# Kernel optimization log

Measured on AMD Instinct MI355X. Metric: run time of the kernel, lower is better.

## Reference

```python
import jax, jax.numpy as jnp
import numpy as np

TOP_K = 2
NUM_EXPERTS = 8

def setup_inputs() -> dict:
    key = jax.random.key(0)
    k_x, k_r, k_g, k_u, k_d = jax.random.split(key, 5)
    B, L, D, H, E = 1, 2048, 1024, 2048, NUM_EXPERTS
    scale = 0.02  # keep router logits / activations in a sane range
    return {
        "x": jax.random.normal(k_x, (B, L, D), dtype=jnp.float32),
        "router_w": jax.random.normal(k_r, (D, E), dtype=jnp.float32) * scale,
        "gate_w": jax.random.normal(k_g, (E, D, H), dtype=jnp.float32) * scale,
        "up_w": jax.random.normal(k_u, (E, D, H), dtype=jnp.float32) * scale,
        "down_w": jax.random.normal(k_d, (E, H, D), dtype=jnp.float32) * scale,
    }

def reference(x, router_w, gate_w, up_w, down_w):
    # x: (B, L, D)
    B, L, D = x.shape
    T = B * L
    E = router_w.shape[1]
    xf = x.reshape(T, D)

    # --- router: top-k softmax over selected logits (Mixtral-style) ---
    logits = xf @ router_w                      # (T, E)
    top_vals, top_idx = jax.lax.top_k(logits, TOP_K)  # (T, K)
    top_w = jax.nn.softmax(top_vals, axis=-1)   # (T, K)

    # combine weights scattered to dense (T, E); zeros for unrouted experts
    combine = jnp.zeros((T, E), dtype=x.dtype).at[
        jnp.arange(T)[:, None], top_idx
    ].add(top_w)

    # --- experts: SwiGLU, computed per expert, zero-weight tokens masked by combine ---
    gate = jnp.einsum('td,edh->eth', xf, gate_w)   # (E, T, H)
    up = jnp.einsum('td,edh->eth', xf, up_w)       # (E, T, H)
    hidden = jax.nn.silu(gate) * up                # (E, T, H)
    expert_out = jnp.einsum('eth,ehd->etd', hidden, down_w)  # (E, T, D)

    # --- weighted combine (equivalent to scatter_add over sorted assignments) ---
    y = jnp.einsum('etd,te->td', expert_out, combine)  # (T, D)
    return y.reshape(B, L, D)
```

## Files before the change

### kernel.cpp

```cpp
#include <hip/hip_runtime.h>
#include <hip/hip_bf16.h>
#include <stdint.h>

#define T_TOK 2048
#define DIM   1024
#define HDIM  2048
#define NE    8
#define ROWS_PAD 4224

typedef __attribute__((ext_vector_type(8))) short bf16x8;
typedef __attribute__((ext_vector_type(4))) float f32x4;

__device__ __forceinline__ unsigned short f2bf(float f) {
    union { float f; unsigned int u; } v; v.f = f;
    unsigned int r = v.u + 0x7FFF + ((v.u >> 16) & 1);
    return (unsigned short)(r >> 16);
}

__device__ __forceinline__ void gload16(const void* g, void* l) {
    __builtin_amdgcn_global_load_lds(
        (const __attribute__((address_space(1))) void*)g,
        (__attribute__((address_space(3))) void*)l, 16, 0, 0);
}

__global__ void transpose_cvt(const float* __restrict__ in, unsigned short* __restrict__ out,
                              int R, int C) {
    __shared__ float tile[32][33];
    int b = blockIdx.z;
    int bx = blockIdx.x, by = blockIdx.y;
    int tx = threadIdx.x & 31, ty = threadIdx.x >> 5;
    const float* ip = in + (size_t)b * R * C;
    unsigned short* op = out + (size_t)b * R * C;
#pragma unroll
    for (int i = 0; i < 4; ++i) {
        int r = by * 32 + ty + i * 8;
        tile[ty + i * 8][tx] = ip[(size_t)r * C + bx * 32 + tx];
    }
    __syncthreads();
#pragma unroll
    for (int i = 0; i < 4; ++i) {
        int oc = bx * 32 + ty + i * 8;
        int orw = by * 32 + tx;
        op[(size_t)oc * R + orw] = f2bf(tile[tx][ty + i * 8]);
    }
}

__global__ void router_kernel(const float* __restrict__ x, const float* __restrict__ rw,
                              int* __restrict__ counts, int* __restrict__ top_idx,
                              float* __restrict__ top_w) {
    int wid = (blockIdx.x * blockDim.x + threadIdx.x) >> 6;
    int lane = threadIdx.x & 63;
    if (wid >= T_TOK) return;
    float acc[NE];
#pragma unroll
    for (int e = 0; e < NE; ++e) acc[e] = 0.f;
    const float* xr = x + (size_t)wid * DIM;
    for (int i = lane; i < DIM; i += 64) {
        float xv = xr[i];
        const float* wr = rw + (size_t)i * NE;
#pragma unroll
        for (int e = 0; e < NE; ++e) acc[e] += xv * wr[e];
    }
#pragma unroll
    for (int off = 32; off; off >>= 1) {
#pragma unroll
        for (int e = 0; e < NE; ++e) acc[e] += __shfl_xor(acc[e], off, 64);
    }
    if (lane == 0) {
        float v0 = -1e30f, v1 = -1e30f; int i0 = 0, i1 = 0;
#pragma unroll
        for (int e = 0; e < NE; ++e) {
            float v = acc[e];
            if (v > v0) { v1 = v0; i1 = i0; v0 = v; i0 = e; }
            else if (v > v1) { v1 = v; i1 = e; }
        }
        float e1 = __expf(v1 - v0);
        float s = 1.f + e1;
        top_idx[wid * 2]     = i0;
        top_idx[wid * 2 + 1] = i1;
        top_w[wid * 2]     = 1.f / s;
        top_w[wid * 2 + 1] = e1 / s;
        atomicAdd(&counts[i0], 1);
        atomicAdd(&counts[i1], 1);
    }
}

__global__ void scan_kernel(const int* __restrict__ counts, int* __restrict__ offsets,
                            int* __restrict__ cursors) {
    if (threadIdx.x == 0) {
        int run = 0;
        for (int e = 0; e < NE; ++e) { offsets[e] = run; cursors[e] = run; run += counts[e]; }
    }
}

__global__ void gather_kernel(const float* __restrict__ x, const int* __restrict__ top_idx,
                              const float* __restrict__ top_w, int* __restrict__ cursors,
                              int* __restrict__ row_tok, float* __restrict__ row_w,
                              unsigned short* __restrict__ Abuf) {
    int t = blockIdx.x;
    __shared__ int pos[2];
    if (threadIdx.x < 2) {
        int k = threadIdx.x;
        int e = top_idx[t * 2 + k];
        int p = atomicAdd(&cursors[e], 1);
        pos[k] = p;
        row_tok[p] = t;
        row_w[p] = top_w[t * 2 + k];
    }
    __syncthreads();
    const float4* xr = (const float4*)(x + (size_t)t * DIM);
    float4 v = xr[threadIdx.x];
    ushort4 b;
    b.x = f2bf(v.x); b.y = f2bf(v.y); b.z = f2bf(v.z); b.w = f2bf(v.w);
    ushort4* A4 = (ushort4*)Abuf;
    A4[(size_t)pos[0] * (DIM / 4) + threadIdx.x] = b;
    A4[(size_t)pos[1] * (DIM / 4) + threadIdx.x] = b;
}

__global__ __launch_bounds__(256, 2)
void gemm1_kernel(const unsigned short* __restrict__ Abuf,
                  const unsigned short* __restrict__ WgT,
                  const unsigned short* __restrict__ WuT,
                  unsigned short* __restrict__ Hbuf,
                  const int* __restrict__ offsets, const int* __restrict__ counts) {
    const int e = blockIdx.z;
    const int cnt = counts[e];
    const int mtile = blockIdx.y;
    if (mtile * 128 >= cnt) return;
    const int n0 = blockIdx.x * 128;
    const int row0 = offsets[e] + mtile * 128;

    __shared__ unsigned short As[2][128 * 32];
    __shared__ unsigned short Bg[2][128 * 32];
    __shared__ unsigned short Bu[2][128 * 32];

    const int tid = threadIdx.x;
    const int lane = tid & 63;
    const int wave = tid >> 6;
    const int wm = wave >> 1, wn = wave & 1;

    f32x4 accg[4][4], accu[4][4];
#pragma unroll
    for (int i = 0; i < 4; ++i)
#pragma unroll
        for (int j = 0; j < 4; ++j) {
            accg[i][j] = (f32x4){0.f, 0.f, 0.f, 0.f};
            accu[i][j] = (f32x4){0.f, 0.f, 0.f, 0.f};
        }

    const int srow0 = tid >> 2;
    const int sc0 = tid & 3;
    const unsigned short* Aab = Abuf + (size_t)row0 * DIM;
    const unsigned short* Bgb = WgT + (size_t)e * HDIM * DIM + (size_t)n0 * DIM;
    const unsigned short* Bub = WuT + (size_t)e * HDIM * DIM + (size_t)n0 * DIM;

    auto stage = [&](int buf, int kt) {
#pragma unroll
        for (int i = 0; i < 2; ++i) {
            int row = i * 64 + srow0;
            int csrc = sc0 ^ ((row >> 1) & 3);
            size_t go = (size_t)row * DIM + kt + csrc * 8;
            int lo = (i * 256 + tid) * 8;
            gload16(Aab + go, &As[buf][lo]);
            gload16(Bgb + go, &Bg[buf][lo]);
            gload16(Bub + go, &Bu[buf][lo]);
        }
    };

    const int rsel = lane & 15;
    const int csrcf = lane >> 4;

    stage(0, 0);
    int cur = 0;
    for (int kt = 0; kt < DIM; kt += 32) {
        __syncthreads();
        if (kt + 32 < DIM) stage(cur ^ 1, kt + 32);
        const unsigned short* Ac = As[cur];
        const unsigned short* Bgc = Bg[cur];
        const unsigned short* Buc = Bu[cur];
        bf16x8 af[4], bg[4], bu[4];
#pragma unroll
        for (int i = 0; i < 4; ++i) {
            int ra = wm * 64 + i * 16 + rsel;
            af[i] = *(const bf16x8*)&Ac[ra * 32 + (csrcf ^ ((ra >> 1) & 3)) * 8];
            int rb = wn * 64 + i * 16 + rsel;
            int cb = (csrcf ^ ((rb >> 1) & 3)) * 8;
            bg[i] = *(const bf16x8*)&Bgc[rb * 32 + cb];
            bu[i] = *(const bf16x8*)&Buc[rb * 32 + cb];
        }
#pragma unroll
        for (int i = 0; i < 4; ++i)
#pragma unroll
            for (int j = 0; j < 4; ++j) {
                accg[i][j] = __builtin_amdgcn_mfma_f32_16x16x32_bf16(af[i], bg[j], accg[i][j], 0, 0, 0);
                accu[i][j] = __builtin_amdgcn_mfma_f32_16x16x32_bf16(af[i], bu[j], accu[i][j], 0, 0, 0);
            }
        cur ^= 1;
    }

    const int c = lane & 15, rbase = (lane >> 4) * 4;
    const int obase = offsets[e];
#pragma unroll
    for (int i = 0; i < 4; ++i) {
#pragma unroll
        for (int r = 0; r < 4; ++r) {
            int lrow = mtile * 128 + wm * 64 + i * 16 + rbase + r;
            if (lrow < cnt) {
                size_t orow = (size_t)(obase + lrow);
#pragma unroll
                for (int j = 0; j < 4; ++j) {
                    float g = accg[i][j][r], u = accu[i][j][r];
                    float h = g * u / (1.f + __expf(-g));
                    Hbuf[orow * HDIM + n0 + wn * 64 + j * 16 + c] = f2bf(h);
                }
            }
        }
    }
}

__global__ __launch_bounds__(256, 2)
void gemm2_kernel(const unsigned short* __restrict__ Hbuf,
                  const unsigned short* __restrict__ WdT,
                  float* __restrict__ y,
                  const int* __restrict__ offsets, const int* __restrict__ counts,
                  const int* __restrict__ row_tok, const float* __restrict__ row_w) {
    const int e = blockIdx.z >> 1;
    const int kc = blockIdx.z & 1;
    const int cnt = counts[e];
    const int mtile = blockIdx.y;
    if (mtile * 128 >= cnt) return;
    const int n0 = blockIdx.x * 128;
    const int row0 = offsets[e] + mtile * 128;

    __shared__ unsigned short As[2][128 * 64];
    __shared__ unsigned short Bs[2][128 * 64];

    const int tid = threadIdx.x;
    const int lane = tid & 63;
    const int wave = tid >> 6;
    const int wm = wave >> 1, wn = wave & 1;

    f32x4 acc[4][4];
#pragma unroll
    for (int i = 0; i < 4; ++i)
#pragma unroll
        for (int j = 0; j < 4; ++j) acc[i][j] = (f32x4){0.f, 0.f, 0.f, 0.f};

    const int srow0 = tid >> 3;
    const int sc0 = tid & 7;
    const unsigned short* Aab = Hbuf + (size_t)row0 * HDIM;
    const unsigned short* Bbb = WdT + (size_t)e * DIM * HDIM + (size_t)n0 * HDIM;

    auto stage = [&](int buf, int kt) {
#pragma unroll
        for (int i = 0; i < 4; ++i) {
            int row = i * 32 + srow0;
            int csrc = sc0 ^ (row & 7);
            size_t go = (size_t)row * HDIM + kt + csrc * 8;
            int lo = (i * 256 + tid) * 8;
            gload16(Aab + go, &As[buf][lo]);
            gload16(Bbb + go, &Bs[buf][lo]);
        }
    };

    const int rsel = lane & 15;
    const int csrcf = lane >> 4;

    const int kbeg = kc * (HDIM / 2);
    const int kend = kbeg + (HDIM / 2);

    stage(0, kbeg);
    int cur = 0;
    for (int kt = kbeg; kt < kend; kt += 64) {
        __syncthreads();
        if (kt + 64 < kend) stage(cur ^ 1, kt + 64);
        const unsigned short* Ac = As[cur];
        const unsigned short* Bc = Bs[cur];
#pragma unroll
        for (int kk = 0; kk < 2; ++kk) {
            bf16x8 af[4], bf[4];
#pragma unroll
            for (int i = 0; i < 4; ++i) {
                int ra = wm * 64 + i * 16 + rsel;
                af[i] = *(const bf16x8*)&Ac[ra * 64 + ((kk * 4 + csrcf) ^ (ra & 7)) * 8];
                int rb = wn * 64 + i * 16 + rsel;
                bf[i] = *(const bf16x8*)&Bc[rb * 64 + ((kk * 4 + csrcf) ^ (rb & 7)) * 8];
            }
#pragma unroll
            for (int i = 0; i < 4; ++i)
#pragma unroll
                for (int j = 0; j < 4; ++j)
                    acc[i][j] = __builtin_amdgcn_mfma_f32_16x16x32_bf16(af[i], bf[j], acc[i][j], 0, 0, 0);
        }
        cur ^= 1;
    }

    const int c = lane & 15, rbase = (lane >> 4) * 4;
    const int obase = offsets[e];
#pragma unroll
    for (int i = 0; i < 4; ++i) {
#pragma unroll
        for (int r = 0; r < 4; ++r) {
            int lrow = mtile * 128 + wm * 64 + i * 16 + rbase + r;
            if (lrow < cnt) {
                int grow = obase + lrow;
                int tok = row_tok[grow];
                float w = row_w[grow];
#pragma unroll
                for (int j = 0; j < 4; ++j) {
                    atomicAdd(&y[(size_t)tok * DIM + n0 + wn * 64 + j * 16 + c], w * acc[i][j][r]);
                }
            }
        }
    }
}

extern "C" void kernel_launch(void* const* d_in, const int* in_sizes, int n_in,
                              void* d_out, int out_size, void* d_ws, size_t ws_size,
                              hipStream_t stream) {
    const float* x  = (const float*)d_in[0];
    const float* rw = (const float*)d_in[1];
    const float* gw = (const float*)d_in[2];
    const float* uw = (const float*)d_in[3];
    const float* dw = (const float*)d_in[4];
    float* y = (float*)d_out;

    char* ws = (char*)d_ws;
    int*   counts  = (int*)(ws + 0);
    int*   cursors = (int*)(ws + 32);
    int*   offsets = (int*)(ws + 64);
    int*   top_idx = (int*)(ws + 128);
    float* top_w   = (float*)(ws + 128 + 16384);
    int*   row_tok = (int*)(ws + 128 + 32768);
    float* row_w   = (float*)(ws + 128 + 32768 + 16896);
    size_t off = 128 + 32768 + 2 * 16896;
    off = (off + 255) & ~(size_t)255;
    unsigned short* Abuf = (unsigned short*)(ws + off); off += (size_t)ROWS_PAD * DIM * 2;
    unsigned short* Hbuf = (unsigned short*)(ws + off); off += (size_t)ROWS_PAD * HDIM * 2;
    unsigned short* WgT  = (unsigned short*)(ws + off); off += (size_t)NE * DIM * HDIM * 2;
    unsigned short* WuT  = (unsigned short*)(ws + off); off += (size_t)NE * DIM * HDIM * 2;
    unsigned short* WdT  = (unsigned short*)(ws + off); off += (size_t)NE * DIM * HDIM * 2;
    if (ws_size < off) return;

    hipMemsetAsync(counts, 0, 32, stream);
    hipMemsetAsync(d_out, 0, (size_t)out_size * 4, stream);

    transpose_cvt<<<dim3(HDIM / 32, DIM / 32, NE), 256, 0, stream>>>(gw, WgT, DIM, HDIM);
    transpose_cvt<<<dim3(HDIM / 32, DIM / 32, NE), 256, 0, stream>>>(uw, WuT, DIM, HDIM);
    transpose_cvt<<<dim3(DIM / 32, HDIM / 32, NE), 256, 0, stream>>>(dw, WdT, HDIM, DIM);

    router_kernel<<<T_TOK / 4, 256, 0, stream>>>(x, rw, counts, top_idx, top_w);
    scan_kernel<<<1, 64, 0, stream>>>(counts, offsets, cursors);
    gather_kernel<<<T_TOK, 256, 0, stream>>>(x, top_idx, top_w, cursors, row_tok, row_w, Abuf);

    gemm1_kernel<<<dim3(HDIM / 128, 16, NE), 256, 0, stream>>>(Abuf, WgT, WuT, Hbuf, offsets, counts);
    gemm2_kernel<<<dim3(DIM / 128, 16, NE * 2), 256, 0, stream>>>(Hbuf, WdT, y, offsets, counts, row_tok, row_w);
}
```

Before: 281.9 us.

## Triple-buffer LDS pipelines in both expert GEMMs with explicit vmcnt waits

Both expert GEMM kernels move from double to triple buffering of shared-memory tiles. Two stages are prefetched ahead, and each iteration waits with an explicit s_waitcnt vmcnt count plus a raw barrier instead of __syncthreads, so global-to-LDS loads can overlap more compute. gemm2 also shrinks its K tile from 64 to 32, which lowers its LDS footprint, and raises its launch bounds to 3 blocks per SM for higher occupancy. Risks: the hand-set vmcnt counts rely on the compiler not adding other outstanding vector memory ops, and the smaller K step in gemm2 doubles the barrier count.

After: 285.5 us. About the same (+1.3%).

```diff
diff --git a/kernel.cpp b/kernel.cpp
--- a/kernel.cpp
+++ b/kernel.cpp
@@ -130,9 +130,9 @@
     const int n0 = blockIdx.x * 128;
     const int row0 = offsets[e] + mtile * 128;
 
-    __shared__ unsigned short As[2][128 * 32];
-    __shared__ unsigned short Bg[2][128 * 32];
-    __shared__ unsigned short Bu[2][128 * 32];
+    __shared__ unsigned short As[3][128 * 32];
+    __shared__ unsigned short Bg[3][128 * 32];
+    __shared__ unsigned short Bu[3][128 * 32];
 
     const int tid = threadIdx.x;
     const int lane = tid & 63;
@@ -170,11 +170,18 @@
     const int rsel = lane & 15;
     const int csrcf = lane >> 4;
 
+    const int NS = DIM / 32;
     stage(0, 0);
+    stage(1, 32);
     int cur = 0;
-    for (int kt = 0; kt < DIM; kt += 32) {
-        __syncthreads();
-        if (kt + 32 < DIM) stage(cur ^ 1, kt + 32);
+    for (int s = 0; s < NS; ++s) {
+        if (s + 1 < NS) { asm volatile("s_waitcnt vmcnt(6)" ::: "memory"); }
+        else            { asm volatile("s_waitcnt vmcnt(0)" ::: "memory"); }
+        __builtin_amdgcn_s_barrier();
+        if (s + 2 < NS) {
+            int pb = cur + 2; if (pb >= 3) pb -= 3;
+            stage(pb, (s + 2) * 32);
+        }
         const unsigned short* Ac = As[cur];
         const unsigned short* Bgc = Bg[cur];
         const unsigned short* Buc = Bu[cur];
@@ -195,7 +202,7 @@
                 accg[i][j] = __builtin_amdgcn_mfma_f32_16x16x32_bf16(af[i], bg[j], accg[i][j], 0, 0, 0);
                 accu[i][j] = __builtin_amdgcn_mfma_f32_16x16x32_bf16(af[i], bu[j], accu[i][j], 0, 0, 0);
             }
-        cur ^= 1;
+        ++cur; if (cur == 3) cur = 0;
     }
 
     const int c = lane & 15, rbase = (lane >> 4) * 4;
@@ -218,7 +225,7 @@
     }
 }
 
-__global__ __launch_bounds__(256, 2)
+__global__ __launch_bounds__(256, 3)
 void gemm2_kernel(const unsigned short* __restrict__ Hbuf,
                   const unsigned short* __restrict__ WdT,
                   float* __restrict__ y,
@@ -232,8 +239,8 @@
     const int n0 = blockIdx.x * 128;
     const int row0 = offsets[e] + mtile * 128;
 
-    __shared__ unsigned short As[2][128 * 64];
-    __shared__ unsigned short Bs[2][128 * 64];
+    __shared__ unsigned short As[3][128 * 32];
+    __shared__ unsigned short Bs[3][128 * 32];
 
     const int tid = threadIdx.x;
     const int lane = tid & 63;
@@ -246,16 +253,16 @@
 #pragma unroll
         for (int j = 0; j < 4; ++j) acc[i][j] = (f32x4){0.f, 0.f, 0.f, 0.f};
 
-    const int srow0 = tid >> 3;
-    const int sc0 = tid & 7;
+    const int srow0 = tid >> 2;
+    const int sc0 = tid & 3;
     const unsigned short* Aab = Hbuf + (size_t)row0 * HDIM;
     const unsigned short* Bbb = WdT + (size_t)e * DIM * HDIM + (size_t)n0 * HDIM;
 
     auto stage = [&](int buf, int kt) {
 #pragma unroll
-        for (int i = 0; i < 4; ++i) {
-            int row = i * 32 + srow0;
-            int csrc = sc0 ^ (row & 7);
+        for (int i = 0; i < 2; ++i) {
+            int row = i * 64 + srow0;
+            int csrc = sc0 ^ ((row >> 1) & 3);
             size_t go = (size_t)row * HDIM + kt + csrc * 8;
             int lo = (i * 256 + tid) * 8;
             gload16(Aab + go, &As[buf][lo]);
@@ -267,32 +274,35 @@
     const int csrcf = lane >> 4;
 
     const int kbeg = kc * (HDIM / 2);
-    const int kend = kbeg + (HDIM / 2);
+    const int NS = (HDIM / 2) / 32;
 
     stage(0, kbeg);
+    stage(1, kbeg + 32);
     int cur = 0;
-    for (int kt = kbeg; kt < kend; kt += 64) {
-        __syncthreads();
-        if (kt + 64 < kend) stage(cur ^ 1, kt + 64);
+    for (int s = 0; s < NS; ++s) {
+        if (s + 1 < NS) { asm volatile("s_waitcnt vmcnt(4)" ::: "memory"); }
+        else            { asm volatile("s_waitcnt vmcnt(0)" ::: "memory"); }
+        __builtin_amdgcn_s_barrier();
+        if (s + 2 < NS) {
+            int pb = cur + 2; if (pb >= 3) pb -= 3;
+            stage(pb, kbeg + (s + 2) * 32);
+        }
         const unsigned short* Ac = As[cur];
         const unsigned short* Bc = Bs[cur];
-#pragma unroll
-        for (int kk = 0; kk < 2; ++kk) {
-            bf16x8 af[4], bf[4];
-#pragma unroll
-            for (int i = 0; i < 4; ++i) {
-                int ra = wm * 64 + i * 16 + rsel;
-                af[i] = *(const bf16x8*)&Ac[ra * 64 + ((kk * 4 + csrcf) ^ (ra & 7)) * 8];
-                int rb = wn * 64 + i * 16 + rsel;
-                bf[i] = *(const bf16x8*)&Bc[rb * 64 + ((kk * 4 + csrcf) ^ (rb & 7)) * 8];
-            }
-#pragma unroll
-            for (int i = 0; i < 4; ++i)
-#pragma unroll
-                for (int j = 0; j < 4; ++j)
-                    acc[i][j] = __builtin_amdgcn_mfma_f32_16x16x32_bf16(af[i], bf[j], acc[i][j], 0, 0, 0);
-        }
-        cur ^= 1;
+        bf16x8 af[4], bf[4];
+#pragma unroll
+        for (int i = 0; i < 4; ++i) {
+            int ra = wm * 64 + i * 16 + rsel;
+            af[i] = *(const bf16x8*)&Ac[ra * 32 + (csrcf ^ ((ra >> 1) & 3)) * 8];
+            int rb = wn * 64 + i * 16 + rsel;
+            bf[i] = *(const bf16x8*)&Bc[rb * 32 + (csrcf ^ ((rb >> 1) & 3)) * 8];
+        }
+#pragma unroll
+        for (int i = 0; i < 4; ++i)
+#pragma unroll
+            for (int j = 0; j < 4; ++j)
+                acc[i][j] = __builtin_amdgcn_mfma_f32_16x16x32_bf16(af[i], bf[j], acc[i][j], 0, 0, 0);
+        ++cur; if (cur == 3) cur = 0;
     }
 
     const int c = lane & 15, rbase = (lane >> 4) * 4;
```
